# Performance work log

Hardware: AMD Instinct MI355X
Metric: run time of the kernel (lower is better)

Reference implementation:

```python
import jax, jax.numpy as jnp
import numpy as np

DILATIONS = [1, 2, 4, 8, 16, 32, 64, 128, 256, 512]
C = 256   # channels
K = 3     # kernel size


def causal_conv(x, w, b, d):
    # x: [B, C_in, T], w: [C_out, C_in, K] -> [B, C_out, T], left-padded causal
    y = jax.lax.conv_general_dilated(
        x, w,
        window_strides=(1,),
        padding=[((K - 1) * d, 0)],
        rhs_dilation=(d,),
        dimension_numbers=('NCH', 'OIH', 'NCH'))
    return y + b[None, :, None]


def setup_inputs() -> dict:
    key = jax.random.key(0)
    ks = jax.random.split(key, 5)
    L = len(DILATIONS)
    B, T = 4, 8192
    s = 0.05  # weight scale
    return {
        'input': jax.random.normal(ks[0], (B, C, T), jnp.float32),
        'weights_conv': jax.random.normal(ks[1], (L, 2 * C, C, K), jnp.float32) * s,
        'biases_conv': jax.random.normal(ks[2], (L, 2 * C), jnp.float32) * s,
        'weights_out': jax.random.normal(ks[3], (L, C, C), jnp.float32) * s,
        'biases_out': jax.random.normal(ks[4], (L, C), jnp.float32) * s,
    }


def reference(input, weights_conv, biases_conv, weights_out, biases_out):
    x = input  # [B, C, T]
    L = len(DILATIONS)
    skips = []
    for i, d in enumerate(DILATIONS):
        z = causal_conv(x, weights_conv[i], biases_conv[i], d)  # [B, 2C, T]
        # gated activation: tanh on first half, sigmoid on second half
        h = jnp.tanh(z[:, :C]) * jax.nn.sigmoid(z[:, C:])       # [B, C, T]
        skips.append(h)
        if i < L - 1:
            # 1x1 output transform (disabled on the last layer)
            out = jnp.einsum('oc,bct->bot', weights_out[i], h) + biases_out[i][None, :, None]
        else:
            out = h
        x = out + x  # residual connection applied in the stack
    return x, jnp.stack(skips, axis=0)  # ([B,C,T], [L,B,C,T])
```

## Files before the change

kernel.cpp:

```cpp
#include <hip/hip_runtime.h>
#include <hip/hip_bf16.h>

#define BATCH 4
#define CCH 256
#define TLEN 8192
#define LAYERS 10
#define BCT (BATCH*CCH*TLEN)
#define TPAD 1024
#define TROWS (TPAD + TLEN)

typedef __attribute__((ext_vector_type(8))) short bf16x8;
typedef __attribute__((ext_vector_type(4))) float f32x4;

__device__ __forceinline__ unsigned short f2b(float f) {
  union { float f; unsigned u; } v; v.f = f;
  unsigned r = (v.u + 0x7FFFu + ((v.u >> 16) & 1u)) >> 16;
  return (unsigned short)r;
}
__device__ __forceinline__ float b2f(unsigned short h) {
  union { unsigned u; float f; } v; v.u = ((unsigned)h) << 16;
  return v.f;
}

__device__ __forceinline__ void gload16(const void* g, void* l) {
  __builtin_amdgcn_global_load_lds((__attribute__((address_space(1))) void*)g,
                                   (__attribute__((address_space(3))) void*)l, 16, 0, 0);
}

__device__ __forceinline__ float fast_tanh(float x) {
  float a = fabsf(x);
  float e = __expf(-2.f * a);
  float th = (1.f - e) * __builtin_amdgcn_rcpf(1.f + e);
  return copysignf(th, x);
}
__device__ __forceinline__ float fast_sigmoid(float x) {
  return __builtin_amdgcn_rcpf(1.f + __expf(-x));
}

__global__ void repack_w(const float* __restrict__ wc, const float* __restrict__ wo,
                         unsigned short* __restrict__ Wb, unsigned short* __restrict__ Wob) {
  size_t g = (size_t)blockIdx.x * 256 + threadIdx.x;
  const size_t NA = (size_t)LAYERS * 3 * 4 * 128 * 256;
  if (g < NA) {
    int c   = (int)(g & 255);
    int row = (int)((g >> 8) & 127);
    int y   = (int)((g >> 15) & 3);
    int lt  = (int)(g >> 17);
    int tap = lt % 3, l = lt / 3;
    int ch = y * 64 + ((row >> 5) << 4) + (row & 15) + (((row >> 4) & 1) << 8);
    Wb[g] = f2b(wc[(((size_t)l * 512 + ch) * 256 + c) * 3 + tap]);
  } else {
    size_t g2 = g - NA;
    if (g2 < (size_t)LAYERS * 256 * 256) Wob[g2] = f2b(wo[g2]);
  }
}

__global__ void zero_pads(unsigned short* __restrict__ xTb) {
  size_t off = (size_t)blockIdx.y * TROWS * CCH;
  int i = blockIdx.x * 256 + threadIdx.x;
  ulonglong2 z; z.x = 0ull; z.y = 0ull;
  ((ulonglong2*)(xTb + off))[i] = z;
}

__global__ void transpose_in(const float* __restrict__ in, float* __restrict__ xT,
                             unsigned short* __restrict__ xTb) {
  __shared__ float tile[32][33];
  const int tid = threadIdx.x;
  const int t0 = blockIdx.x * 32, c0 = blockIdx.y * 32, b = blockIdx.z;
#pragma unroll
  for (int q = 0; q < 4; ++q) {
    int e = tid + 256 * q; int r = e >> 5, cc = e & 31;
    tile[r][cc] = in[((size_t)b * CCH + c0 + r) * TLEN + t0 + cc];
  }
  __syncthreads();
#pragma unroll
  for (int q = 0; q < 4; ++q) {
    int e = tid + 256 * q; int r = e >> 5, cc = e & 31;
    float v = tile[cc][r];
    xT[((size_t)b * TLEN + t0 + r) * CCH + c0 + cc] = v;
    xTb[((size_t)b * TROWS + TPAD + t0 + r) * CCH + c0 + cc] = f2b(v);
  }
}

__global__ void final_addT(const float* __restrict__ xT, const unsigned short* __restrict__ hT,
                           float* __restrict__ out) {
  __shared__ float tile[32][33];
  const int tid = threadIdx.x;
  const int t0 = blockIdx.x * 32, c0 = blockIdx.y * 32, b = blockIdx.z;
#pragma unroll
  for (int q = 0; q < 4; ++q) {
    int e = tid + 256 * q; int r = e >> 5, cc = e & 31;
    size_t idx = ((size_t)b * TLEN + t0 + r) * CCH + c0 + cc;
    tile[r][cc] = xT[idx] + b2f(hT[idx]);
  }
  __syncthreads();
#pragma unroll
  for (int q = 0; q < 4; ++q) {
    int e = tid + 256 * q; int r = e >> 5, cc = e & 31;
    out[((size_t)b * CCH + c0 + r) * TLEN + t0 + cc] = tile[cc][r];
  }
}

__global__ __launch_bounds__(256)
void conv_gate_kernel(const unsigned short* __restrict__ xTb,
                      const unsigned short* __restrict__ Wl,
                      const float* __restrict__ bias,
                      unsigned short* __restrict__ hT,
                      float* __restrict__ skip,
                      int d) {
  __shared__ unsigned short As[2][128 * 32];
  __shared__ unsigned short Bs[2][128 * 32];

  const int tid  = threadIdx.x;
  const int lane = tid & 63;
  const int wv   = tid >> 6;
  const int wm   = wv & 1, wn = wv >> 1;
  const int col  = lane & 15, quad = lane >> 4;

  const int t0 = blockIdx.x * 128;
  const int y  = blockIdx.y;
  const int o0 = y * 64;
  const int b  = blockIdx.z;

  const int rl = lane >> 2;
  const int kl = (lane & 3) * 8;
  const int ch0 = wv * 2;

  const unsigned short* Arow = xTb + ((size_t)b * TROWS + TPAD + t0) * CCH;

  f32x4 acc[4][4];
  const f32x4 zero = {0.f, 0.f, 0.f, 0.f};
#pragma unroll
  for (int i = 0; i < 4; ++i)
#pragma unroll
    for (int j = 0; j < 4; ++j) acc[i][j] = zero;

  const int NCHUNK = 24;

  auto stage = [&](int idx, int buf) {
    const int tap = idx >> 3;
    const int c0  = (idx & 7) << 5;
    const unsigned short* Ab = Arow - (size_t)((2 - tap) * d) * CCH;
    const unsigned short* Wb = Wl + ((size_t)tap * 4 + y) * (128 * 256);
    gload16(Ab + (size_t)(ch0 * 16      + rl) * CCH + c0 + kl, &As[buf][ ch0      * 512]);
    gload16(Ab + (size_t)(ch0 * 16 + 16 + rl) * CCH + c0 + kl, &As[buf][(ch0 + 1) * 512]);
    gload16(Wb + (size_t)(ch0 * 16      + rl) * 256 + c0 + kl, &Bs[buf][ ch0      * 512]);
    gload16(Wb + (size_t)(ch0 * 16 + 16 + rl) * 256 + c0 + kl, &Bs[buf][(ch0 + 1) * 512]);
  };

  auto step = [&](int buf, int next_idx) {
    const int k0 = quad * 8;
    bf16x8 af[4], bfv[4];
#pragma unroll
    for (int mf = 0; mf < 4; ++mf)
      af[mf] = *(const bf16x8*)&As[buf][(wm * 64 + mf * 16 + col) * 32 + k0];
#pragma unroll
    for (int nf = 0; nf < 4; ++nf)
      bfv[nf] = *(const bf16x8*)&Bs[buf][(wn * 64 + nf * 16 + col) * 32 + k0];
    if (next_idx < NCHUNK) stage(next_idx, buf ^ 1);
#pragma unroll
    for (int mf = 0; mf < 4; ++mf)
#pragma unroll
      for (int nf = 0; nf < 4; ++nf)
        acc[mf][nf] = __builtin_amdgcn_mfma_f32_16x16x32_bf16(af[mf], bfv[nf], acc[mf][nf], 0, 0, 0);
  };

  stage(0, 0);
  __syncthreads();
#pragma unroll 1
  for (int i = 0; i < NCHUNK; i += 2) {
    step(0, i + 1); __syncthreads();
    step(1, i + 2); __syncthreads();
  }

#pragma unroll
  for (int mf = 0; mf < 4; ++mf) {
    const int tb = t0 + wm * 64 + mf * 16 + quad * 4;
#pragma unroll
    for (int p = 0; p < 2; ++p) {
      const int pair = wn * 2 + p;
      const int ch = o0 + pair * 16 + col;
      const float btop = bias[ch];
      const float bbot = bias[ch + 256];
      f32x4 zt = acc[mf][2 * p];
      f32x4 zb = acc[mf][2 * p + 1];
      float hr[4];
#pragma unroll
      for (int r = 0; r < 4; ++r) {
        float h = fast_tanh(zt[r] + btop) * fast_sigmoid(zb[r] + bbot);
        hr[r] = h;
        hT[((size_t)b * TLEN + tb + r) * CCH + ch] = f2b(h);
      }
      float4 hv; hv.x = hr[0]; hv.y = hr[1]; hv.z = hr[2]; hv.w = hr[3];
      *(float4*)&skip[((size_t)b * CCH + ch) * TLEN + tb] = hv;
    }
  }
}

__global__ __launch_bounds__(256)
void onexone_kernel(const unsigned short* __restrict__ hT,
                    const unsigned short* __restrict__ Wo,
                    const float* __restrict__ bias,
                    float* __restrict__ xT,
                    unsigned short* __restrict__ xTb) {
  __shared__ unsigned short As[2][128 * 32];
  __shared__ unsigned short Bs[2][128 * 32];

  const int tid  = threadIdx.x;
  const int lane = tid & 63;
  const int wv   = tid >> 6;
  const int wm   = wv & 1, wn = wv >> 1;
  const int col  = lane & 15, quad = lane >> 4;

  const int t0 = blockIdx.x * 128;
  const int o0 = blockIdx.y * 128;
  const int b  = blockIdx.z;

  const int rl = lane >> 2;
  const int kl = (lane & 3) * 8;
  const int ch0 = wv * 2;

  const unsigned short* Ab = hT + (size_t)b * TLEN * CCH + (size_t)t0 * CCH;
  const unsigned short* Wb = Wo + (size_t)o0 * 256;

  f32x4 acc[4][4];
  const f32x4 zero = {0.f, 0.f, 0.f, 0.f};
#pragma unroll
  for (int i = 0; i < 4; ++i)
#pragma unroll
    for (int j = 0; j < 4; ++j) acc[i][j] = zero;

  const int NCHUNK = 8;

  auto stage = [&](int idx, int buf) {
    const int c0 = idx << 5;
    gload16(Ab + (size_t)(ch0 * 16      + rl) * CCH + c0 + kl, &As[buf][ ch0      * 512]);
    gload16(Ab + (size_t)(ch0 * 16 + 16 + rl) * CCH + c0 + kl, &As[buf][(ch0 + 1) * 512]);
    gload16(Wb + (size_t)(ch0 * 16      + rl) * 256 + c0 + kl, &Bs[buf][ ch0      * 512]);
    gload16(Wb + (size_t)(ch0 * 16 + 16 + rl) * 256 + c0 + kl, &Bs[buf][(ch0 + 1) * 512]);
  };

  auto step = [&](int buf, int next_idx) {
    const int k0 = quad * 8;
    bf16x8 af[4], bfv[4];
#pragma unroll
    for (int mf = 0; mf < 4; ++mf)
      af[mf] = *(const bf16x8*)&As[buf][(wm * 64 + mf * 16 + col) * 32 + k0];
#pragma unroll
    for (int nf = 0; nf < 4; ++nf)
      bfv[nf] = *(const bf16x8*)&Bs[buf][(wn * 64 + nf * 16 + col) * 32 + k0];
    if (next_idx < NCHUNK) stage(next_idx, buf ^ 1);
#pragma unroll
    for (int mf = 0; mf < 4; ++mf)
#pragma unroll
      for (int nf = 0; nf < 4; ++nf)
        acc[mf][nf] = __builtin_amdgcn_mfma_f32_16x16x32_bf16(af[mf], bfv[nf], acc[mf][nf], 0, 0, 0);
  };

  stage(0, 0);
  __syncthreads();
#pragma unroll 1
  for (int i = 0; i < NCHUNK; i += 2) {
    step(0, i + 1); __syncthreads();
    step(1, i + 2); __syncthreads();
  }

#pragma unroll
  for (int mf = 0; mf < 4; ++mf) {
    const int tb = t0 + wm * 64 + mf * 16 + quad * 4;
#pragma unroll
    for (int nf = 0; nf < 4; ++nf) {
      const int ch = o0 + wn * 64 + nf * 16 + col;
      const float bo = bias[ch];
#pragma unroll
      for (int r = 0; r < 4; ++r) {
        size_t idx = ((size_t)b * TLEN + tb + r) * CCH + ch;
        float nv = xT[idx] + acc[mf][nf][r] + bo;
        xT[idx] = nv;
        xTb[((size_t)b * TROWS + TPAD + tb + r) * CCH + ch] = f2b(nv);
      }
    }
  }
}

extern "C" void kernel_launch(void* const* d_in, const int* in_sizes, int n_in,
                              void* d_out, int out_size, void* d_ws, size_t ws_size,
                              hipStream_t stream) {
  const float* input = (const float*)d_in[0];
  const float* wconv = (const float*)d_in[1];
  const float* bconv = (const float*)d_in[2];
  const float* wout  = (const float*)d_in[3];
  const float* bout  = (const float*)d_in[4];
  float* out   = (float*)d_out;
  float* skips = out + (size_t)BCT;

  char* ws = (char*)d_ws;
  float*          xT  = (float*)ws;
  unsigned short* xTb = (unsigned short*)(ws + (size_t)BCT * 4);
  unsigned short* hT  = (unsigned short*)(ws + (size_t)BCT * 4
                                             + (size_t)BATCH * TROWS * CCH * 2);
  unsigned short* Wb  = hT + (size_t)BCT;
  unsigned short* Wob = Wb + (size_t)LAYERS * 3 * 512 * 256;

  static const int dil[LAYERS] = {1, 2, 4, 8, 16, 32, 64, 128, 256, 512};

  repack_w<<<17920, 256, 0, stream>>>(wconv, wout, Wb, Wob);
  zero_pads<<<dim3(128, BATCH), 256, 0, stream>>>(xTb);
  transpose_in<<<dim3(TLEN / 32, CCH / 32, BATCH), 256, 0, stream>>>(input, xT, xTb);

  for (int l = 0; l < LAYERS; ++l) {
    conv_gate_kernel<<<dim3(TLEN / 128, 4, BATCH), 256, 0, stream>>>(
        xTb, Wb + (size_t)l * 3 * 512 * 256, bconv + (size_t)l * 512,
        hT, skips + (size_t)l * BCT, dil[l]);
    if (l < LAYERS - 1) {
      onexone_kernel<<<dim3(TLEN / 128, 2, BATCH), 256, 0, stream>>>(
          hT, Wob + (size_t)l * 256 * 256, bout + (size_t)l * 256, xT, xTb);
    } else {
      final_addT<<<dim3(TLEN / 32, CCH / 32, BATCH), 256, 0, stream>>>(xT, hT, out);
    }
  }
}
```

Baseline: 1.061 ms.

## Enlarge conv-gate tile to 256x256 with triple-buffered swizzled LDS pipeline

The dilated conv + gate kernel now uses 512-thread blocks computing a 256-time by 128-channel-pair tile, instead of 128x64. Each block stages A and B through three LDS buffers, waiting on vmcnt rather than block-wide __syncthreads. LDS rows are XOR-swizzled to avoid bank conflicts, blocks are remapped for locality, and s_setprio raises priority around the MFMA bursts. The weight repack is changed to the new 256-row layout. The aim is more data reuse per byte loaded and better overlap of loads with MFMA, at the cost of about 96KB of LDS per block, which limits occupancy, and a grid of only 256 blocks.

New measurement: 981.9 us. 7.5% less time.

```diff
diff --git a/kernel.cpp b/kernel.cpp
--- a/kernel.cpp
+++ b/kernel.cpp
@@ -40,14 +40,14 @@
 __global__ void repack_w(const float* __restrict__ wc, const float* __restrict__ wo,
                          unsigned short* __restrict__ Wb, unsigned short* __restrict__ Wob) {
   size_t g = (size_t)blockIdx.x * 256 + threadIdx.x;
-  const size_t NA = (size_t)LAYERS * 3 * 4 * 128 * 256;
+  const size_t NA = (size_t)LAYERS * 3 * 2 * 256 * 256;
   if (g < NA) {
     int c   = (int)(g & 255);
-    int row = (int)((g >> 8) & 127);
-    int y   = (int)((g >> 15) & 3);
+    int row = (int)((g >> 8) & 255);
+    int y   = (int)((g >> 16) & 1);
     int lt  = (int)(g >> 17);
     int tap = lt % 3, l = lt / 3;
-    int ch = y * 64 + ((row >> 5) << 4) + (row & 15) + (((row >> 4) & 1) << 8);
+    int ch = y * 128 + ((row >> 5) << 4) + (row & 15) + (((row >> 4) & 1) << 8);
     Wb[g] = f2b(wc[(((size_t)l * 512 + ch) * 256 + c) * 3 + tap]);
   } else {
     size_t g2 = g - NA;
@@ -101,87 +101,128 @@
   }
 }
 
-__global__ __launch_bounds__(256)
+__global__ __launch_bounds__(512, 2)
 void conv_gate_kernel(const unsigned short* __restrict__ xTb,
                       const unsigned short* __restrict__ Wl,
                       const float* __restrict__ bias,
                       unsigned short* __restrict__ hT,
                       float* __restrict__ skip,
                       int d) {
-  __shared__ unsigned short As[2][128 * 32];
-  __shared__ unsigned short Bs[2][128 * 32];
+  __shared__ __align__(16) unsigned short As[3][256 * 32];
+  __shared__ __align__(16) unsigned short Bs[3][256 * 32];
 
   const int tid  = threadIdx.x;
   const int lane = tid & 63;
   const int wv   = tid >> 6;
-  const int wm   = wv & 1, wn = wv >> 1;
+  const int wm   = wv & 1;
+  const int wn   = wv >> 1;
   const int col  = lane & 15, quad = lane >> 4;
 
-  const int t0 = blockIdx.x * 128;
-  const int y  = blockIdx.y;
-  const int o0 = y * 64;
-  const int b  = blockIdx.z;
-
-  const int rl = lane >> 2;
-  const int kl = (lane & 3) * 8;
-  const int ch0 = wv * 2;
+  const int bid  = blockIdx.x;
+  const int swzb = (bid & 7) * 32 + (bid >> 3);
+  const int t0   = (swzb & 31) * 256;
+  const int y    = (swzb >> 5) & 1;
+  const int b    = swzb >> 6;
+
+  const int srow  = lane >> 2;
+  const int sslot = lane & 3;
 
   const unsigned short* Arow = xTb + ((size_t)b * TROWS + TPAD + t0) * CCH;
 
-  f32x4 acc[4][4];
+  f32x4 acc[8][4];
   const f32x4 zero = {0.f, 0.f, 0.f, 0.f};
 #pragma unroll
-  for (int i = 0; i < 4; ++i)
+  for (int i = 0; i < 8; ++i)
 #pragma unroll
     for (int j = 0; j < 4; ++j) acc[i][j] = zero;
 
-  const int NCHUNK = 24;
-
-  auto stage = [&](int idx, int buf) {
-    const int tap = idx >> 3;
-    const int c0  = (idx & 7) << 5;
-    const unsigned short* Ab = Arow - (size_t)((2 - tap) * d) * CCH;
-    const unsigned short* Wb = Wl + ((size_t)tap * 4 + y) * (128 * 256);
-    gload16(Ab + (size_t)(ch0 * 16      + rl) * CCH + c0 + kl, &As[buf][ ch0      * 512]);
-    gload16(Ab + (size_t)(ch0 * 16 + 16 + rl) * CCH + c0 + kl, &As[buf][(ch0 + 1) * 512]);
-    gload16(Wb + (size_t)(ch0 * 16      + rl) * 256 + c0 + kl, &Bs[buf][ ch0      * 512]);
-    gload16(Wb + (size_t)(ch0 * 16 + 16 + rl) * 256 + c0 + kl, &Bs[buf][(ch0 + 1) * 512]);
-  };
-
-  auto step = [&](int buf, int next_idx) {
-    const int k0 = quad * 8;
-    bf16x8 af[4], bfv[4];
+  const int NT = 24;
+
+  auto stageA = [&](int kt, int slot) {
+    const int tap = kt >> 3, c0 = (kt & 7) << 5;
+    const unsigned short* Ab = Arow - (size_t)((2 - tap) * d) * CCH + c0;
+#pragma unroll
+    for (int j = 0; j < 2; ++j) {
+      const int row = (wv * 2 + j) * 16 + srow;
+      const int ss  = sslot ^ ((row >> 1) & 3);
+      gload16(Ab + (size_t)row * CCH + ss * 8, &As[slot][(wv * 2 + j) * 512]);
+    }
+  };
+  auto stageB = [&](int kt, int slot) {
+    const int tap = kt >> 3, c0 = (kt & 7) << 5;
+    const unsigned short* Wp = Wl + ((size_t)(tap * 2 + y)) * (256 * 256) + c0;
+#pragma unroll
+    for (int j = 0; j < 2; ++j) {
+      const int row = (wv * 2 + j) * 16 + srow;
+      const int ss  = sslot ^ ((row >> 1) & 3);
+      gload16(Wp + (size_t)row * 256 + ss * 8, &Bs[slot][(wv * 2 + j) * 512]);
+    }
+  };
+
+  auto ktile = [&](int slot, int stageKt, bool vm4) {
+    if (vm4) asm volatile("s_waitcnt vmcnt(4)" ::: "memory");
+    else     asm volatile("s_waitcnt vmcnt(0)" ::: "memory");
+    __builtin_amdgcn_s_barrier();
+    const int pslot = (slot + 2) % 3;
+    bf16x8 bf[4], af[4];
+#pragma unroll
+    for (int nf = 0; nf < 4; ++nf) {
+      const int row = wn * 64 + nf * 16 + col;
+      bf[nf] = *(const bf16x8*)&Bs[slot][row * 32 + ((quad ^ ((row >> 1) & 3)) << 3)];
+    }
+#pragma unroll
+    for (int mf = 0; mf < 4; ++mf) {
+      const int row = wm * 128 + mf * 16 + col;
+      af[mf] = *(const bf16x8*)&As[slot][row * 32 + ((quad ^ ((row >> 1) & 3)) << 3)];
+    }
+    if (stageKt >= 0) stageA(stageKt, pslot);
+    __builtin_amdgcn_s_setprio(1);
 #pragma unroll
     for (int mf = 0; mf < 4; ++mf)
-      af[mf] = *(const bf16x8*)&As[buf][(wm * 64 + mf * 16 + col) * 32 + k0];
-#pragma unroll
-    for (int nf = 0; nf < 4; ++nf)
-      bfv[nf] = *(const bf16x8*)&Bs[buf][(wn * 64 + nf * 16 + col) * 32 + k0];
-    if (next_idx < NCHUNK) stage(next_idx, buf ^ 1);
+#pragma unroll
+      for (int nf = 0; nf < 4; ++nf)
+        acc[mf][nf] = __builtin_amdgcn_mfma_f32_16x16x32_bf16(af[mf], bf[nf], acc[mf][nf], 0, 0, 0);
+    __builtin_amdgcn_s_setprio(0);
+    __builtin_amdgcn_sched_barrier(0);
+#pragma unroll
+    for (int mf = 0; mf < 4; ++mf) {
+      const int row = wm * 128 + (mf + 4) * 16 + col;
+      af[mf] = *(const bf16x8*)&As[slot][row * 32 + ((quad ^ ((row >> 1) & 3)) << 3)];
+    }
+    if (stageKt >= 0) stageB(stageKt, pslot);
+    __builtin_amdgcn_s_setprio(1);
 #pragma unroll
     for (int mf = 0; mf < 4; ++mf)
 #pragma unroll
       for (int nf = 0; nf < 4; ++nf)
-        acc[mf][nf] = __builtin_amdgcn_mfma_f32_16x16x32_bf16(af[mf], bfv[nf], acc[mf][nf], 0, 0, 0);
-  };
-
-  stage(0, 0);
-  __syncthreads();
+        acc[mf + 4][nf] = __builtin_amdgcn_mfma_f32_16x16x32_bf16(af[mf], bf[nf], acc[mf + 4][nf], 0, 0, 0);
+    __builtin_amdgcn_s_setprio(0);
+    asm volatile("s_waitcnt lgkmcnt(0)" ::: "memory");
+    __builtin_amdgcn_sched_barrier(0);
+  };
+
+  stageA(0, 0); stageB(0, 0);
+  stageA(1, 1); stageB(1, 1);
+
 #pragma unroll 1
-  for (int i = 0; i < NCHUNK; i += 2) {
-    step(0, i + 1); __syncthreads();
-    step(1, i + 2); __syncthreads();
-  }
-
-#pragma unroll
-  for (int mf = 0; mf < 4; ++mf) {
-    const int tb = t0 + wm * 64 + mf * 16 + quad * 4;
-#pragma unroll
-    for (int p = 0; p < 2; ++p) {
-      const int pair = wn * 2 + p;
-      const int ch = o0 + pair * 16 + col;
-      const float btop = bias[ch];
-      const float bbot = bias[ch + 256];
+  for (int kt = 0; kt < 21; kt += 3) {
+    ktile(0, kt + 2, true);
+    ktile(1, kt + 3, true);
+    ktile(2, kt + 4, true);
+  }
+  ktile(0, 23, true);
+  ktile(1, -1, true);
+  ktile(2, -1, false);
+
+#pragma unroll
+  for (int p = 0; p < 2; ++p) {
+    const int chn = y * 128 + (wn * 2 + p) * 16 + col;
+    const float btop = bias[chn];
+    const float bbot = bias[chn + 256];
+    const size_t skipBase = ((size_t)b * CCH + chn) * TLEN;
+#pragma unroll
+    for (int mf = 0; mf < 8; ++mf) {
+      const int tb = t0 + wm * 128 + mf * 16 + quad * 4;
       f32x4 zt = acc[mf][2 * p];
       f32x4 zb = acc[mf][2 * p + 1];
       float hr[4];
@@ -189,10 +230,10 @@
       for (int r = 0; r < 4; ++r) {
         float h = fast_tanh(zt[r] + btop) * fast_sigmoid(zb[r] + bbot);
         hr[r] = h;
-        hT[((size_t)b * TLEN + tb + r) * CCH + ch] = f2b(h);
+        hT[((size_t)b * TLEN + tb + r) * CCH + chn] = f2b(h);
       }
       float4 hv; hv.x = hr[0]; hv.y = hr[1]; hv.z = hr[2]; hv.w = hr[3];
-      *(float4*)&skip[((size_t)b * CCH + ch) * TLEN + tb] = hv;
+      *(float4*)&skip[skipBase + tb] = hv;
     }
   }
 }
@@ -309,7 +350,7 @@
   transpose_in<<<dim3(TLEN / 32, CCH / 32, BATCH), 256, 0, stream>>>(input, xT, xTb);
 
   for (int l = 0; l < LAYERS; ++l) {
-    conv_gate_kernel<<<dim3(TLEN / 128, 4, BATCH), 256, 0, stream>>>(
+    conv_gate_kernel<<<256, 512, 0, stream>>>(
         xTb, Wb + (size_t)l * 3 * 512 * 256, bconv + (size_t)l * 512,
         hT, skips + (size_t)l * BCT, dil[l]);
     if (l < LAYERS - 1) {
```
